# Optimization experiments

Measured on AMD Instinct MI355X. Metric: run time of the kernel, lower is better.

Reference implementation:

```python
import jax, jax.numpy as jnp
import numpy as np

N, D, H, C, K, NCLS, TW = 8192, 768, 4, 192, 8, 7, 1.0
HC = H * C  # 768


def setup_inputs() -> dict:
    key = jax.random.key(0)
    ks = jax.random.split(key, 40)
    gl = lambda i, shp: (jax.random.normal(ks[i], shp, jnp.float32)
                         * (1.0 / np.sqrt(shp[0] if len(shp) > 1 else shp[0])))
    inp = {"x": jax.random.normal(ks[0], (N, D), jnp.float32)}
    # BatchNorm (eval mode: running stats)
    inp["bn_gamma"] = jnp.ones((D,), jnp.float32)
    inp["bn_beta"] = jnp.zeros((D,), jnp.float32)
    inp["bn_rm"] = jnp.zeros((D,), jnp.float32)
    inp["bn_rv"] = jnp.ones((D,), jnp.float32)
    # GATConv params: W [in, H*C], att_src/att_dst [H, C], bias
    dims_in = [D, HC, HC, C]
    bias_dim = [HC, HC, C, C]  # concat,concat,mean,mean
    for li in range(4):
        b = 1 + li * 3
        inp[f"g{li+1}_w"] = gl(b, (dims_in[li], HC))
        inp[f"g{li+1}_as"] = jax.random.normal(ks[b + 1], (H, C), jnp.float32) * 0.1
        inp[f"g{li+1}_ad"] = jax.random.normal(ks[b + 2], (H, C), jnp.float32) * 0.1
        inp[f"g{li+1}_b"] = jnp.zeros((bias_dim[li],), jnp.float32)
    inp["res1_w"] = gl(14, (D, HC)); inp["res1_b"] = jnp.zeros((HC,), jnp.float32)
    inp["res2_w"] = gl(15, (HC, C)); inp["res2_b"] = jnp.zeros((C,), jnp.float32)
    for li, dim in zip(range(4), [HC, HC, C, C]):
        inp[f"ln{li+1}_g"] = jnp.ones((dim,), jnp.float32)
        inp[f"ln{li+1}_b"] = jnp.zeros((dim,), jnp.float32)
    inp["fc_w"] = gl(16, (C, NCLS)); inp["fc_b"] = jnp.zeros((NCLS,), jnp.float32)
    return inp


def _ln(x, g, b):
    mu = x.mean(-1, keepdims=True)
    v = ((x - mu) ** 2).mean(-1, keepdims=True)
    return (x - mu) * jax.lax.rsqrt(v + 1e-5) * g + b


def _build_edges(x):
    # cosine-similarity top-k graph (indices only; grads are cut upstream,
    # matching the original .item()-based host loop)
    xn = x / (jnp.linalg.norm(x, axis=1, keepdims=True) + 1e-8)
    sim = xn @ xn.T                       # [N, N]
    _, idx = jax.lax.top_k(sim, K + 1)    # first hit is self
    nbr = idx[:, 1:]                      # [N, K]
    src0 = jnp.repeat(jnp.arange(N), K)
    dst0 = nbr.reshape(-1)
    i = jnp.arange(N - 1)
    # temporal edges (i,i+1)&(i+1,i) added only if (i,i+1) not already a topk edge
    m = ~jnp.any(nbr[:-1] == (i + 1)[:, None], axis=1)
    sl = jnp.arange(N)  # self-loops (GATConv add_self_loops=True)
    src = jnp.concatenate([src0, i, i + 1, sl])
    dst = jnp.concatenate([dst0, i + 1, i, sl])
    mask = jnp.concatenate([jnp.ones(N * K, bool), m, m, jnp.ones(N, bool)])
    return src, dst, mask


def _gat(x, W, a_s, a_d, b, src, dst, mask, concat):
    n = x.shape[0]
    h = (x @ W).reshape(n, H, C)
    es = (h * a_s[None]).sum(-1)  # [N, H]
    ed = (h * a_d[None]).sum(-1)
    e = jax.nn.leaky_relu(es[src] + ed[dst], 0.2)  # [E, H]
    e = jnp.where(mask[:, None], e, -1e9)
    emax = jax.ops.segment_max(e, dst, num_segments=n)
    emax = jnp.where(jnp.isfinite(emax), emax, 0.0)
    ex = jnp.exp(e - emax[dst]) * mask[:, None].astype(e.dtype)
    denom = jax.ops.segment_sum(ex, dst, num_segments=n)
    alpha = ex / (denom[dst] + 1e-16)
    out = jax.ops.segment_sum(alpha[:, :, None] * h[src], dst, num_segments=n)
    out = out.reshape(n, HC) if concat else out.mean(1)
    return out + b


def reference(x, bn_gamma, bn_beta, bn_rm, bn_rv,
              g1_w, g1_as, g1_ad, g1_b, g2_w, g2_as, g2_ad, g2_b,
              g3_w, g3_as, g3_ad, g3_b, g4_w, g4_as, g4_ad, g4_b,
              res1_w, res1_b, res2_w, res2_b,
              ln1_g, ln1_b, ln2_g, ln2_b, ln3_g, ln3_b, ln4_g, ln4_b,
              fc_w, fc_b):
    xb = (x - bn_rm) * jax.lax.rsqrt(bn_rv + 1e-5) * bn_gamma + bn_beta
    src, dst, mask = _build_edges(jax.lax.stop_gradient(xb))
    r = xb @ res1_w + res1_b
    h = _gat(xb, g1_w, g1_as, g1_ad, g1_b, src, dst, mask, True)
    h = _ln(jax.nn.relu(h) + r, ln1_g, ln1_b)
    r = h
    h = _gat(h, g2_w, g2_as, g2_ad, g2_b, src, dst, mask, True)
    h = _ln(jax.nn.relu(h) + r, ln2_g, ln2_b)
    r = h @ res2_w + res2_b
    h = _gat(h, g3_w, g3_as, g3_ad, g3_b, src, dst, mask, False)
    h = _ln(jax.nn.relu(h) + r, ln3_g, ln3_b)
    r = h
    h = _gat(h, g4_w, g4_as, g4_ad, g4_b, src, dst, mask, False)
    h = _ln(jax.nn.relu(h) + r, ln4_g, ln4_b)
    return h @ fc_w + fc_b
```

## Files before the change

### kernel.cpp

```cpp
#include <hip/hip_runtime.h>
#include <hip/hip_bf16.h>

#define NN 8192
#define DD 768
#define HH 4
#define CC 192
#define KK 8
#define HC 768

typedef __attribute__((ext_vector_type(8))) short short8;
typedef __attribute__((ext_vector_type(4))) float floatx4;

static __device__ __forceinline__ short f2bf(float v) {
    unsigned u = __builtin_bit_cast(unsigned, v);
    u += 0x7fff + ((u >> 16) & 1);
    return (short)(u >> 16);
}
static __device__ __forceinline__ float bf2f(short s) {
    unsigned u = ((unsigned)(unsigned short)s) << 16;
    return __builtin_bit_cast(float, u);
}

static __device__ __forceinline__ void gl16(const void* g, void* l) {
    __builtin_amdgcn_global_load_lds(
        (__attribute__((address_space(1))) void*)(void*)g,
        (__attribute__((address_space(3))) void*)l, 16, 0, 0);
}

__global__ __launch_bounds__(256) void bnorm_kernel(const float* __restrict__ x,
    const float* __restrict__ g, const float* __restrict__ b,
    const float* __restrict__ rm, const float* __restrict__ rv,
    short* __restrict__ xbh, short* __restrict__ xbl,
    short* __restrict__ xnh, short* __restrict__ xnl)
{
    int i = blockIdx.x, t = threadIdx.x;
    __shared__ float red[256];
    float v[3];
    float ss = 0.f;
#pragma unroll
    for (int q = 0; q < 3; q++) {
        int d = t + q * 256;
        float xv = x[(size_t)i * DD + d];
        float vv = (xv - rm[d]) * rsqrtf(rv[d] + 1e-5f) * g[d] + b[d];
        v[q] = vv; ss += vv * vv;
    }
    red[t] = ss; __syncthreads();
    for (int s = 128; s; s >>= 1) { if (t < s) red[t] += red[t + s]; __syncthreads(); }
    float inv = 1.0f / (sqrtf(red[0]) + 1e-8f);
#pragma unroll
    for (int q = 0; q < 3; q++) {
        int d = t + q * 256;
        size_t idx = (size_t)i * DD + d;
        float vv = v[q];
        short h = f2bf(vv);
        xbh[idx] = h; xbl[idx] = f2bf(vv - bf2f(h));
        float nv = vv * inv;
        short nh = f2bf(nv);
        xnh[idx] = nh; xnl[idx] = f2bf(nv - bf2f(nh));
    }
}

__global__ __launch_bounds__(256) void wtrans(const float* __restrict__ w,
    short* __restrict__ whi, short* __restrict__ wlo, int K, int P)
{
    int idx = blockIdx.x * 256 + threadIdx.x;
    if (idx >= K * P) return;
    int p = idx / K, k = idx % K;
    float v = w[(size_t)k * P + p];
    short h = f2bf(v);
    whi[idx] = h;
    wlo[idx] = f2bf(v - bf2f(h));
}

__global__ __launch_bounds__(256) void mfma_nt(
    const short* __restrict__ Ahi, const short* __restrict__ Alo,
    const short* __restrict__ Bhi, const short* __restrict__ Blo,
    const float* __restrict__ bias, int biasN, float* __restrict__ C,
    int M, int K, int P, int Cstride)
{
    __shared__ __attribute__((aligned(16))) short sAh[128 * 32];
    __shared__ __attribute__((aligned(16))) short sAl[128 * 32];
    __shared__ __attribute__((aligned(16))) short sBh[128 * 32];
    __shared__ __attribute__((aligned(16))) short sBl[128 * 32];
    int t = threadIdx.x;
    int wave = t >> 6, lane = t & 63;
    int wm = wave & 1, wn = wave >> 1;
    int i0 = blockIdx.y * 128, j0 = blockIdx.x * 128;
    int mrow = lane & 15, quad = lane >> 4;

    int srow = lane >> 2;
    int kg   = (lane & 3) ^ ((lane >> 3) & 3);
    int koff = kg * 8;
    int c0 = wave * 2, c1 = c0 + 1;
    int ar0 = i0 + c0 * 16 + srow, ar1 = i0 + c1 * 16 + srow;
    int br0 = j0 + c0 * 16 + srow, br1 = j0 + c1 * 16 + srow;
    if (br0 > P - 1) br0 = P - 1;
    if (br1 > P - 1) br1 = P - 1;
    const short* pAh0 = Ahi + (size_t)ar0 * K + koff;
    const short* pAh1 = Ahi + (size_t)ar1 * K + koff;
    const short* pAl0 = Alo + (size_t)ar0 * K + koff;
    const short* pAl1 = Alo + (size_t)ar1 * K + koff;
    const short* pBh0 = Bhi + (size_t)br0 * K + koff;
    const short* pBh1 = Bhi + (size_t)br1 * K + koff;
    const short* pBl0 = Blo + (size_t)br0 * K + koff;
    const short* pBl1 = Blo + (size_t)br1 * K + koff;
    short* dA0 = sAh + c0 * 512; short* dA1 = sAh + c1 * 512;
    short* dAl0 = sAl + c0 * 512; short* dAl1 = sAl + c1 * 512;
    short* dB0 = sBh + c0 * 512; short* dB1 = sBh + c1 * 512;
    short* dBl0 = sBl + c0 * 512; short* dBl1 = sBl + c1 * 512;

    floatx4 acc[4][4];
#pragma unroll
    for (int a = 0; a < 4; a++)
#pragma unroll
        for (int b = 0; b < 4; b++) acc[a][b] = (floatx4){0.f, 0.f, 0.f, 0.f};

    int aoff[4], boff[4];
#pragma unroll
    for (int mt = 0; mt < 4; mt++) {
        int r = wm * 64 + mt * 16 + mrow;
        aoff[mt] = r * 32 + (quad ^ ((r >> 1) & 3)) * 8;
    }
#pragma unroll
    for (int nt = 0; nt < 4; nt++) {
        int r = wn * 64 + nt * 16 + mrow;
        boff[nt] = r * 32 + (quad ^ ((r >> 1) & 3)) * 8;
    }

    for (int k0 = 0; k0 < K; k0 += 32) {
        gl16(pAh0 + k0, dA0);  gl16(pAh1 + k0, dA1);
        gl16(pAl0 + k0, dAl0); gl16(pAl1 + k0, dAl1);
        gl16(pBh0 + k0, dB0);  gl16(pBh1 + k0, dB1);
        gl16(pBl0 + k0, dBl0); gl16(pBl1 + k0, dBl1);
        __syncthreads();

        short8 ah[4], al[4], bh[4], bl[4];
#pragma unroll
        for (int mt = 0; mt < 4; mt++) {
            ah[mt] = *(const short8*)(sAh + aoff[mt]);
            al[mt] = *(const short8*)(sAl + aoff[mt]);
        }
#pragma unroll
        for (int nt = 0; nt < 4; nt++) {
            bh[nt] = *(const short8*)(sBh + boff[nt]);
            bl[nt] = *(const short8*)(sBl + boff[nt]);
        }
#pragma unroll
        for (int mt = 0; mt < 4; mt++)
#pragma unroll
            for (int nt = 0; nt < 4; nt++) {
                acc[mt][nt] = __builtin_amdgcn_mfma_f32_16x16x32_bf16(
                    ah[mt], bh[nt], acc[mt][nt], 0, 0, 0);
                acc[mt][nt] = __builtin_amdgcn_mfma_f32_16x16x32_bf16(
                    ah[mt], bl[nt], acc[mt][nt], 0, 0, 0);
                acc[mt][nt] = __builtin_amdgcn_mfma_f32_16x16x32_bf16(
                    al[mt], bh[nt], acc[mt][nt], 0, 0, 0);
            }
        __syncthreads();
    }

#pragma unroll
    for (int mt = 0; mt < 4; mt++)
#pragma unroll
        for (int nt = 0; nt < 4; nt++) {
            int col = j0 + wn * 64 + nt * 16 + mrow;
            if (col < P) {
                float bb = (bias && col < biasN) ? bias[col] : 0.f;
#pragma unroll
                for (int r = 0; r < 4; r++) {
                    int row = i0 + wm * 64 + mt * 16 + quad * 4 + r;
                    C[(size_t)row * Cstride + col] = acc[mt][nt][r] + bb;
                }
            }
        }
}

__device__ __forceinline__ bool tk_try(float* v, int* id, float xv, int xi)
{
    if (xv > v[8] || (xv == v[8] && xi < id[8])) {
        v[8] = xv; id[8] = xi;
#pragma unroll
        for (int p = 8; p > 0; p--) {
            if (v[p] > v[p - 1] || (v[p] == v[p - 1] && id[p] < id[p - 1])) {
                float tv = v[p]; v[p] = v[p - 1]; v[p - 1] = tv;
                int ti2 = id[p]; id[p] = id[p - 1]; id[p - 1] = ti2;
            } else break;
        }
        return true;
    }
    return false;
}

__global__ __launch_bounds__(256) void topk1_kernel(const float* __restrict__ sim,
    float* __restrict__ pv, int* __restrict__ pi)
{
    int wave = threadIdx.x >> 6, lane = threadIdx.x & 63;
    int task = blockIdx.x * 4 + wave;
    int row = task >> 3, seg = task & 7;
    const float4* p4 = (const float4*)(sim + (size_t)row * NN + seg * 1024);

    float4 f0 = p4[lane], f1 = p4[lane + 64], f2 = p4[lane + 128], f3 = p4[lane + 192];
    float v[9]; int id[9];
#pragma unroll
    for (int q = 0; q < 9; q++) { v[q] = -3e38f; id[q] = 0x7fffffff; }
    int jb = seg * 1024 + lane * 4;
#pragma unroll
    for (int g = 0; g < 4; g++) {
        float4 f = g == 0 ? f0 : (g == 1 ? f1 : (g == 2 ? f2 : f3));
        float gm = fmaxf(fmaxf(f.x, f.y), fmaxf(f.z, f.w));
        if (gm >= v[8]) {
            int j = jb + g * 256;
            tk_try(v, id, f.x, j);
            tk_try(v, id, f.y, j + 1);
            tk_try(v, id, f.z, j + 2);
            tk_try(v, id, f.w, j + 3);
        }
    }
    float wv = -3e38f; int wi = 0x7fffffff;
#pragma unroll
    for (int r = 0; r < 9; r++) {
        float bv = v[0]; int bi = id[0];
#pragma unroll
        for (int off = 1; off < 64; off <<= 1) {
            float ov = __shfl_xor(bv, off);
            int oi = __shfl_xor(bi, off);
            if (ov > bv || (ov == bv && oi < bi)) { bv = ov; bi = oi; }
        }
        if (id[0] == bi) {
#pragma unroll
            for (int q = 0; q < 8; q++) { v[q] = v[q + 1]; id[q] = id[q + 1]; }
            v[8] = -3e38f; id[8] = 0x7fffffff;
        }
        if (lane == r) { wv = bv; wi = bi; }
    }
    if (lane < 9) {
        size_t o = (size_t)task * 9 + lane;
        pv[o] = wv; pi[o] = wi;
    }
}

__global__ __launch_bounds__(256) void topk2_kernel(const float* __restrict__ pv,
    const int* __restrict__ pi, int* __restrict__ nbr, int r0)
{
    int wave = threadIdx.x >> 6, lane = threadIdx.x & 63;
    int row = blockIdx.x * 4 + wave;
    size_t base = (size_t)row * 72;
    float v[2]; int id[2];
    v[0] = -3e38f; id[0] = 0x7fffffff;
    v[1] = -3e38f; id[1] = 0x7fffffff;
    if (lane < 72) { v[0] = pv[base + lane]; id[0] = pi[base + lane]; }
    if (lane < 8)  { v[1] = pv[base + 64 + lane]; id[1] = pi[base + 64 + lane]; }
    if (v[1] > v[0] || (v[1] == v[0] && id[1] < id[0])) {
        float tv = v[0]; v[0] = v[1]; v[1] = tv;
        int ti = id[0]; id[0] = id[1]; id[1] = ti;
    }
    int myi = 0;
#pragma unroll
    for (int r = 0; r < 9; r++) {
        float bv = v[0]; int bi = id[0];
#pragma unroll
        for (int off = 1; off < 64; off <<= 1) {
            float ov = __shfl_xor(bv, off);
            int oi = __shfl_xor(bi, off);
            if (ov > bv || (ov == bv && oi < bi)) { bv = ov; bi = oi; }
        }
        if (id[0] == bi) {
            v[0] = v[1]; id[0] = id[1];
            v[1] = -3e38f; id[1] = 0x7fffffff;
        }
        if (r >= 1 && lane == r - 1) myi = bi;
    }
    if (lane < KK) nbr[(size_t)(r0 + row) * KK + lane] = myi;
}

__global__ __launch_bounds__(256) void count_kernel(const int* __restrict__ nbr,
                                                    int* __restrict__ deg, int* __restrict__ mfl)
{
    int i = blockIdx.x * 256 + threadIdx.x;
    if (i >= NN) return;
    atomicAdd(&deg[i], 1);
    int mm = 0;
#pragma unroll
    for (int k = 0; k < KK; k++) {
        int j = nbr[i * KK + k];
        atomicAdd(&deg[j], 1);
        if (j == i + 1) mm = 1;
    }
    if (i < NN - 1) {
        mfl[i] = !mm;
        if (!mm) { atomicAdd(&deg[i + 1], 1); atomicAdd(&deg[i], 1); }
    }
}

__global__ __launch_bounds__(256) void scan_kernel(const int* __restrict__ deg,
                                                   int* __restrict__ rowptr, int* __restrict__ cur)
{
    __shared__ int sums[256];
    int t = threadIdx.x;
    int loc[32];
    int base = t * 32;
    int s = 0;
#pragma unroll
    for (int q = 0; q < 32; q++) { loc[q] = s; s += deg[base + q]; }
    sums[t] = s; __syncthreads();
    for (int off = 1; off < 256; off <<= 1) {
        int v = (t >= off) ? sums[t - off] : 0;
        __syncthreads();
        sums[t] += v;
        __syncthreads();
    }
    int myoff = (t == 0) ? 0 : sums[t - 1];
#pragma unroll
    for (int q = 0; q < 32; q++) { int rp = myoff + loc[q]; rowptr[base + q] = rp; cur[base + q] = rp; }
    if (t == 255) rowptr[NN] = sums[255];
}

__global__ __launch_bounds__(256) void fill_kernel(const int* __restrict__ nbr,
    const int* __restrict__ mfl, int* __restrict__ cur, int* __restrict__ csr)
{
    int i = blockIdx.x * 256 + threadIdx.x;
    if (i >= NN) return;
    int pos = atomicAdd(&cur[i], 1); csr[pos] = i;
#pragma unroll
    for (int k = 0; k < KK; k++) {
        int j = nbr[i * KK + k];
        pos = atomicAdd(&cur[j], 1); csr[pos] = i;
    }
    if (i < NN - 1 && mfl[i]) {
        pos = atomicAdd(&cur[i + 1], 1); csr[pos] = i;
        pos = atomicAdd(&cur[i], 1); csr[pos] = i + 1;
    }
}

__global__ __launch_bounds__(256) void esed_kernel(const float* __restrict__ h, int hst,
    const float* __restrict__ a_s, const float* __restrict__ a_d,
    float* __restrict__ es, float* __restrict__ ed)
{
    int i = blockIdx.x;
    int t = threadIdx.x;
    int w = t >> 6, lane = t & 63;
    const float* hr = h + (size_t)i * hst + w * CC;
    float ps = 0.f, pd = 0.f;
    for (int c = lane; c < CC; c += 64) {
        float x = hr[c];
        ps += x * a_s[w * CC + c];
        pd += x * a_d[w * CC + c];
    }
#pragma unroll
    for (int off = 32; off; off >>= 1) { ps += __shfl_down(ps, off); pd += __shfl_down(pd, off); }
    if (lane == 0) { es[i * HH + w] = ps; ed[i * HH + w] = pd; }
}

__global__ __launch_bounds__(256) void agg_ln_kernel(const float* __restrict__ h, int hst,
    const float* __restrict__ es, const float* __restrict__ ed,
    const int* __restrict__ rowptr, const int* __restrict__ csr,
    const float* __restrict__ gb, const float* __restrict__ rres, int rst,
    const float* __restrict__ gamma, const float* __restrict__ beta,
    float* __restrict__ outp, short* __restrict__ ohi, short* __restrict__ olo,
    int Dm, int concat,
    const float* __restrict__ fcw, const float* __restrict__ fcb,
    float* __restrict__ fco)
{
    int j = blockIdx.x;
    int t = threadIdx.x;
    int lane = t & 63, wave = t >> 6;
    __shared__ int ssrc[256];
    __shared__ float sal[256 * 4];
    __shared__ float sred[1024];
    __shared__ float accs[768];
    int p0 = rowptr[j], p1 = rowptr[j + 1];
    int cnt = p1 - p0;
    float edj[4];
#pragma unroll
    for (int hd = 0; hd < 4; hd++) edj[hd] = ed[j * 4 + hd];

    float acc0 = 0.f, acc1 = 0.f, acc2 = 0.f;
    int d0 = t, d1 = t + 256, d2 = t + 512;
    int h0 = d0 / CC, h1_ = d1 / CC, h2_ = d2 / CC;

    if (cnt <= 256) {
        float e[4];
        if (t < cnt) {
            int s = csr[p0 + t];
            ssrc[t] = s;
#pragma unroll
            for (int hd = 0; hd < 4; hd++) {
                float ee = es[s * 4 + hd] + edj[hd];
                e[hd] = ee > 0.f ? ee : 0.2f * ee;
            }
        } else {
#pragma unroll
            for (int hd = 0; hd < 4; hd++) e[hd] = -1e30f;
        }
        float mh[4];
#pragma unroll
        for (int hd = 0; hd < 4; hd++) {
            float rv = e[hd];
#pragma unroll
            for (int off = 32; off; off >>= 1) rv = fmaxf(rv, __shfl_down(rv, off));
            if (lane == 0) sred[wave * 4 + hd] = rv;
        }
        __syncthreads();
#pragma unroll
        for (int hd = 0; hd < 4; hd++)
            mh[hd] = fmaxf(fmaxf(sred[hd], sred[4 + hd]), fmaxf(sred[8 + hd], sred[12 + hd]));
        __syncthreads();
        float ex[4];
#pragma unroll
        for (int hd = 0; hd < 4; hd++) {
            ex[hd] = (t < cnt) ? expf(e[hd] - mh[hd]) : 0.f;
            float rv = ex[hd];
#pragma unroll
            for (int off = 32; off; off >>= 1) rv += __shfl_down(rv, off);
            if (lane == 0) sred[wave * 4 + hd] = rv;
        }
        __syncthreads();
#pragma unroll
        for (int hd = 0; hd < 4; hd++) {
            float dh = sred[hd] + sred[4 + hd] + sred[8 + hd] + sred[12 + hd] + 1e-16f;
            if (t < cnt) sal[t * 4 + hd] = ex[hd] / dh;
        }
        __syncthreads();
        for (int e2 = 0; e2 < cnt; e2++) {
            const float* hs = h + (size_t)ssrc[e2] * hst;
            acc0 += sal[e2 * 4 + h0] * hs[d0];
            acc1 += sal[e2 * 4 + h1_] * hs[d1];
            acc2 += sal[e2 * 4 + h2_] * hs[d2];
        }
    } else {
        float mh[4] = {-1e30f, -1e30f, -1e30f, -1e30f};
        for (int p = p0 + t; p < p1; p += 256) {
            int s = csr[p];
#pragma unroll
            for (int hd = 0; hd < 4; hd++) {
                float e = es[s * 4 + hd] + edj[hd];
                e = e > 0.f ? e : 0.2f * e;
                mh[hd] = fmaxf(mh[hd], e);
            }
        }
#pragma unroll
        for (int hd = 0; hd < 4; hd++) sred[hd * 256 + t] = mh[hd];
        __syncthreads();
        for (int s2 = 128; s2; s2 >>= 1) {
            if (t < s2)
#pragma unroll
                for (int hd = 0; hd < 4; hd++)
                    sred[hd * 256 + t] = fmaxf(sred[hd * 256 + t], sred[hd * 256 + t + s2]);
            __syncthreads();
        }
#pragma unroll
        for (int hd = 0; hd < 4; hd++) mh[hd] = sred[hd * 256];
        __syncthreads();
        float sh[4] = {0.f, 0.f, 0.f, 0.f};
        for (int p = p0 + t; p < p1; p += 256) {
            int s = csr[p];
#pragma unroll
            for (int hd = 0; hd < 4; hd++) {
                float e = es[s * 4 + hd] + edj[hd];
                e = e > 0.f ? e : 0.2f * e;
                sh[hd] += expf(e - mh[hd]);
            }
        }
#pragma unroll
        for (int hd = 0; hd < 4; hd++) sred[hd * 256 + t] = sh[hd];
        __syncthreads();
        for (int s2 = 128; s2; s2 >>= 1) {
            if (t < s2)
#pragma unroll
                for (int hd = 0; hd < 4; hd++)
                    sred[hd * 256 + t] += sred[hd * 256 + t + s2];
            __syncthreads();
        }
        float dh[4];
#pragma unroll
        for (int hd = 0; hd < 4; hd++) dh[hd] = sred[hd * 256] + 1e-16f;
        __syncthreads();
        for (int p = p0; p < p1; p += 64) {
            int cn = min(64, p1 - p);
            if (t < cn) {
                int s = csr[p + t];
                ssrc[t] = s;
#pragma unroll
                for (int hd = 0; hd < 4; hd++) {
                    float e = es[s * 4 + hd] + edj[hd];
                    e = e > 0.f ? e : 0.2f * e;
                    sal[t * 4 + hd] = expf(e - mh[hd]) / dh[hd];
                }
            }
            __syncthreads();
            for (int e2 = 0; e2 < cn; e2++) {
                const float* hs = h + (size_t)ssrc[e2] * hst;
                acc0 += sal[e2 * 4 + h0] * hs[d0];
                acc1 += sal[e2 * 4 + h1_] * hs[d1];
                acc2 += sal[e2 * 4 + h2_] * hs[d2];
            }
            __syncthreads();
        }
    }

    if (concat) {
        float v0 = fmaxf(acc0 + gb[d0], 0.f) + rres[(size_t)j * rst + d0];
        float v1 = fmaxf(acc1 + gb[d1], 0.f) + rres[(size_t)j * rst + d1];
        float v2 = fmaxf(acc2 + gb[d2], 0.f) + rres[(size_t)j * rst + d2];
        __syncthreads();
        sred[t] = v0 + v1 + v2; __syncthreads();
        for (int s = 128; s; s >>= 1) { if (t < s) sred[t] += sred[t + s]; __syncthreads(); }
        float mu = sred[0] / 768.f;
        __syncthreads();
        float a0 = v0 - mu, a1 = v1 - mu, a2 = v2 - mu;
        sred[t] = a0 * a0 + a1 * a1 + a2 * a2; __syncthreads();
        for (int s = 128; s; s >>= 1) { if (t < s) sred[t] += sred[t + s]; __syncthreads(); }
        float rs = rsqrtf(sred[0] / 768.f + 1e-5f);
        size_t base = (size_t)j * 768;
        float w0 = a0 * rs * gamma[d0] + beta[d0];
        float w1 = a1 * rs * gamma[d1] + beta[d1];
        float w2 = a2 * rs * gamma[d2] + beta[d2];
        outp[base + d0] = w0; outp[base + d1] = w1; outp[base + d2] = w2;
        short hh;
        hh = f2bf(w0); ohi[base + d0] = hh; olo[base + d0] = f2bf(w0 - bf2f(hh));
        hh = f2bf(w1); ohi[base + d1] = hh; olo[base + d1] = f2bf(w1 - bf2f(hh));
        hh = f2bf(w2); ohi[base + d2] = hh; olo[base + d2] = f2bf(w2 - bf2f(hh));
    } else {
        accs[d0] = acc0; accs[d1] = acc1; accs[d2] = acc2;
        __syncthreads();
        float val = 0.f;
        if (t < CC)
            val = fmaxf((accs[t] + accs[t + CC] + accs[t + 2 * CC] + accs[t + 3 * CC]) * 0.25f
                        + gb[t], 0.f) + rres[(size_t)j * rst + t];
        __syncthreads();
        sred[t] = (t < CC) ? val : 0.f; __syncthreads();
        for (int s = 128; s; s >>= 1) { if (t < s) sred[t] += sred[t + s]; __syncthreads(); }
        float mu = sred[0] / (float)CC;
        __syncthreads();
        float a = val - mu;
        sred[t] = (t < CC) ? a * a : 0.f; __syncthreads();
        for (int s = 128; s; s >>= 1) { if (t < s) sred[t] += sred[t + s]; __syncthreads(); }
        float rs = rsqrtf(sred[0] / (float)CC + 1e-5f);
        float w = a * rs * ((t < CC) ? gamma[t] : 0.f) + ((t < CC) ? beta[t] : 0.f);
        if (t < CC) {
            size_t idx = (size_t)j * CC + t;
            if (outp) outp[idx] = w;
            if (ohi) {
                short hh = f2bf(w);
                ohi[idx] = hh; olo[idx] = f2bf(w - bf2f(hh));
            }
            accs[t] = w;
        }
        if (fco) {
            __syncthreads();
            if (t < 64) {
#pragma unroll
                for (int n = 0; n < 7; n++) {
                    float p = 0.f;
                    for (int d = t; d < CC; d += 64) p += accs[d] * fcw[d * 7 + n];
#pragma unroll
                    for (int off = 32; off; off >>= 1) p += __shfl_down(p, off);
                    if (t == 0) fco[(size_t)j * 7 + n] = p + fcb[n];
                }
            }
        }
    }
}

extern "C" void kernel_launch(void* const* d_in, const int* in_sizes, int n_in,
                              void* d_out, int out_size, void* d_ws, size_t ws_size,
                              hipStream_t stream)
{
    const float* x     = (const float*)d_in[0];
    const float* bn_g  = (const float*)d_in[1];
    const float* bn_b  = (const float*)d_in[2];
    const float* bn_rm = (const float*)d_in[3];
    const float* bn_rv = (const float*)d_in[4];
    const float* g_w[4]  = {(const float*)d_in[5], (const float*)d_in[9],
                            (const float*)d_in[13], (const float*)d_in[17]};
    const float* g_as[4] = {(const float*)d_in[6], (const float*)d_in[10],
                            (const float*)d_in[14], (const float*)d_in[18]};
    const float* g_ad[4] = {(const float*)d_in[7], (const float*)d_in[11],
                            (const float*)d_in[15], (const float*)d_in[19]};
    const float* g_b[4]  = {(const float*)d_in[8], (const float*)d_in[12],
                            (const float*)d_in[16], (const float*)d_in[20]};
    const float* res1_w = (const float*)d_in[21];
    const float* res1_b = (const float*)d_in[22];
    const float* res2_w = (const float*)d_in[23];
    const float* res2_b = (const float*)d_in[24];
    const float* ln_g[4] = {(const float*)d_in[25], (const float*)d_in[27],
                            (const float*)d_in[29], (const float*)d_in[31]};
    const float* ln_b[4] = {(const float*)d_in[26], (const float*)d_in[28],
                            (const float*)d_in[30], (const float*)d_in[32]};
    const float* fc_w = (const float*)d_in[33];
    const float* fc_b = (const float*)d_in[34];
    float* out = (float*)d_out;

    float* F = (float*)d_ws;
    float* ASIM = F; F += 16777216;
    float* H1   = F; F += 6291456;
    float* HB24 = F; F += 6291456;
    float* H2   = F; F += 6291456;
    float* H3   = F; F += 1572864;
    float* ES   = F; F += 32768;
    float* ED   = F; F += 32768;
    short* S = (short*)F;
    short* XNH = S; S += 6291456;
    short* XNL = S; S += 6291456;
    short* XAH = S; S += 6291456;
    short* XAL = S; S += 6291456;
    short* WT1H = S; S += 1179648;
    short* WT1L = S; S += 1179648;
    short* WT2H = S; S += 589824;
    short* WT2L = S; S += 589824;
    short* WT3H = S; S += 737280;
    short* WT3L = S; S += 737280;
    short* WT4H = S; S += 147456;
    short* WT4L = S; S += 147456;
    int* I = (int*)S;
    int* NBR    = I; I += NN * KK;
    int* DEG    = I; I += NN;
    int* ROWPTR = I; I += NN + 8;
    int* CUR    = I; I += NN;
    int* MFL    = I; I += NN;
    int* CSR    = I; I += 131072;
    float* PV   = (float*)I; I += 147456;
    int* PI     = I; I += 147456;

    bnorm_kernel<<<NN, 256, 0, stream>>>(x, bn_g, bn_b, bn_rm, bn_rv,
                                         XAH, XAL, XNH, XNL);
    wtrans<<<(DD * HC + 255) / 256, 256, 0, stream>>>(res1_w, WT1H, WT1L, DD, HC);
    wtrans<<<(DD * HC + 255) / 256, 256, 0, stream>>>(g_w[0], WT1H + 768 * 768, WT1L + 768 * 768, DD, HC);
    wtrans<<<(HC * HC + 255) / 256, 256, 0, stream>>>(g_w[1], WT2H, WT2L, HC, HC);
    wtrans<<<(HC * CC + 255) / 256, 256, 0, stream>>>(res2_w, WT3H, WT3L, HC, CC);
    wtrans<<<(HC * HC + 255) / 256, 256, 0, stream>>>(g_w[2], WT3H + 192 * 768, WT3L + 192 * 768, HC, HC);
    wtrans<<<(CC * HC + 255) / 256, 256, 0, stream>>>(g_w[3], WT4H, WT4L, CC, HC);
    for (int ch = 0; ch < 4; ch++) {
        mfma_nt<<<dim3(NN / 128, 2048 / 128), 256, 0, stream>>>(
            XNH + (size_t)ch * 2048 * DD, XNL + (size_t)ch * 2048 * DD,
            XNH, XNL, nullptr, 0, ASIM, 2048, DD, NN, NN);
        topk1_kernel<<<4096, 256, 0, stream>>>(ASIM, PV, PI);
        topk2_kernel<<<512, 256, 0, stream>>>(PV, PI, NBR, ch * 2048);
    }
    hipMemsetAsync(DEG, 0, NN * sizeof(int), stream);
    count_kernel<<<NN / 256, 256, 0, stream>>>(NBR, DEG, MFL);
    scan_kernel<<<1, 256, 0, stream>>>(DEG, ROWPTR, CUR);
    fill_kernel<<<NN / 256, 256, 0, stream>>>(NBR, MFL, CUR, CSR);
    float* HB1 = ASIM;
    mfma_nt<<<dim3(12, NN / 128), 256, 0, stream>>>(XAH, XAL, WT1H, WT1L,
        res1_b, 768, HB1, NN, DD, 1536, 1536);
    esed_kernel<<<NN, 256, 0, stream>>>(HB1 + 768, 1536, g_as[0], g_ad[0], ES, ED);
    agg_ln_kernel<<<NN, 256, 0, stream>>>(HB1 + 768, 1536, ES, ED, ROWPTR, CSR,
        g_b[0], HB1, 1536, ln_g[0], ln_b[0], H1, XAH, XAL, HC, 1, nullptr, nullptr, nullptr);
    mfma_nt<<<dim3(6, NN / 128), 256, 0, stream>>>(XAH, XAL, WT2H, WT2L,
        nullptr, 0, HB24, NN, HC, HC, HC);
    esed_kernel<<<NN, 256, 0, stream>>>(HB24, HC, g_as[1], g_ad[1], ES, ED);
    agg_ln_kernel<<<NN, 256, 0, stream>>>(HB24, HC, ES, ED, ROWPTR, CSR,
        g_b[1], H1, HC, ln_g[1], ln_b[1], H2, XAH, XAL, HC, 1, nullptr, nullptr, nullptr);
    float* HB3 = ASIM;
    mfma_nt<<<dim3(8, NN / 128), 256, 0, stream>>>(XAH, XAL, WT3H, WT3L,
        res2_b, 192, HB3, NN, HC, 960, 960);
    esed_kernel<<<NN, 256, 0, stream>>>(HB3 + 192, 960, g_as[2], g_ad[2], ES, ED);
    agg_ln_kernel<<<NN, 256, 0, stream>>>(HB3 + 192, 960, ES, ED, ROWPTR, CSR,
        g_b[2], HB3, 960, ln_g[2], ln_b[2], H3, XAH, XAL, CC, 0, nullptr, nullptr, nullptr);
    mfma_nt<<<dim3(6, NN / 128), 256, 0, stream>>>(XAH, XAL, WT4H, WT4L,
        nullptr, 0, HB24, NN, CC, HC, HC);
    esed_kernel<<<NN, 256, 0, stream>>>(HB24, HC, g_as[3], g_ad[3], ES, ED);
    agg_ln_kernel<<<NN, 256, 0, stream>>>(HB24, HC, ES, ED, ROWPTR, CSR,
        g_b[3], H3, CC, ln_g[3], ln_b[3], nullptr, nullptr, nullptr, CC, 0, fc_w, fc_b, out);
}
```

Baseline: 1.224 ms.

## Fuse similarity GEMM with per-tile top-k and merge weight transposes

The cosine-similarity GEMM now does a per-128-column-tile top-9 selection in its epilogue through shared memory, so the full NxN similarity matrix is never written to or re-read from global memory. The four chunked GEMM/topk1/topk2 launches become one fused kernel plus one final merge over 64 tile candidates per row. Six weight-transpose launches are also merged into a single kernel. The cost is a heavier epilogue, with serialized shuffle-based reductions per row inside the GEMM, and a larger candidate merge in topk2.

```diff
diff --git a/kernel.cpp b/kernel.cpp
--- a/kernel.cpp
+++ b/kernel.cpp
@@ -60,16 +60,28 @@
     }
 }
 
-__global__ __launch_bounds__(256) void wtrans(const float* __restrict__ w,
-    short* __restrict__ whi, short* __restrict__ wlo, int K, int P)
+__global__ __launch_bounds__(256) void wtrans6(
+    const float* w0, short* o0h, short* o0l,
+    const float* w1, short* o1h, short* o1l,
+    const float* w2, short* o2h, short* o2l,
+    const float* w3, short* o3h, short* o3l,
+    const float* w4, short* o4h, short* o4l,
+    const float* w5, short* o5h, short* o5l)
 {
     int idx = blockIdx.x * 256 + threadIdx.x;
-    if (idx >= K * P) return;
-    int p = idx / K, k = idx % K;
+    const float* w; short* oh; short* ol; int K, P; int r;
+    if (idx < 589824)            { w = w0; oh = o0h; ol = o0l; K = 768; P = 768; r = idx; }
+    else if (idx < 2 * 589824)   { w = w1; oh = o1h; ol = o1l; K = 768; P = 768; r = idx - 589824; }
+    else if (idx < 3 * 589824)   { w = w2; oh = o2h; ol = o2l; K = 768; P = 768; r = idx - 2 * 589824; }
+    else if (idx < 3 * 589824 + 147456) { w = w3; oh = o3h; ol = o3l; K = 768; P = 192; r = idx - 3 * 589824; }
+    else if (idx < 4 * 589824 + 147456) { w = w4; oh = o4h; ol = o4l; K = 768; P = 768; r = idx - 3 * 589824 - 147456; }
+    else if (idx < 4 * 589824 + 2 * 147456) { w = w5; oh = o5h; ol = o5l; K = 192; P = 768; r = idx - 4 * 589824 - 147456; }
+    else return;
+    int p = r / K, k = r % K;
     float v = w[(size_t)k * P + p];
     short h = f2bf(v);
-    whi[idx] = h;
-    wlo[idx] = f2bf(v - bf2f(h));
+    oh[r] = h;
+    ol[r] = f2bf(v - bf2f(h));
 }
 
 __global__ __launch_bounds__(256) void mfma_nt(
@@ -175,48 +187,148 @@
         }
 }
 
-__device__ __forceinline__ bool tk_try(float* v, int* id, float xv, int xi)
-{
-    if (xv > v[8] || (xv == v[8] && xi < id[8])) {
-        v[8] = xv; id[8] = xi;
-#pragma unroll
-        for (int p = 8; p > 0; p--) {
-            if (v[p] > v[p - 1] || (v[p] == v[p - 1] && id[p] < id[p - 1])) {
-                float tv = v[p]; v[p] = v[p - 1]; v[p - 1] = tv;
-                int ti2 = id[p]; id[p] = id[p - 1]; id[p - 1] = ti2;
-            } else break;
-        }
-        return true;
-    }
-    return false;
-}
-
-__global__ __launch_bounds__(256) void topk1_kernel(const float* __restrict__ sim,
+__global__ __launch_bounds__(256) void mfma_topk(
+    const short* __restrict__ Xh, const short* __restrict__ Xl,
     float* __restrict__ pv, int* __restrict__ pi)
 {
+    __shared__ __attribute__((aligned(16))) short smem[16384];
+    short* sAh = smem;
+    short* sAl = smem + 4096;
+    short* sBh = smem + 8192;
+    short* sBl = smem + 12288;
+    int t = threadIdx.x;
+    int wave = t >> 6, lane = t & 63;
+    int wm = wave & 1, wn = wave >> 1;
+    int i0 = blockIdx.y * 128, j0 = blockIdx.x * 128;
+    int mrow = lane & 15, quad = lane >> 4;
+
+    int srow = lane >> 2;
+    int kg   = (lane & 3) ^ ((lane >> 3) & 3);
+    int koff = kg * 8;
+    int c0 = wave * 2, c1 = c0 + 1;
+    int ar0 = i0 + c0 * 16 + srow, ar1 = i0 + c1 * 16 + srow;
+    int br0 = j0 + c0 * 16 + srow, br1 = j0 + c1 * 16 + srow;
+    const short* pAh0 = Xh + (size_t)ar0 * DD + koff;
+    const short* pAh1 = Xh + (size_t)ar1 * DD + koff;
+    const short* pAl0 = Xl + (size_t)ar0 * DD + koff;
+    const short* pAl1 = Xl + (size_t)ar1 * DD + koff;
+    const short* pBh0 = Xh + (size_t)br0 * DD + koff;
+    const short* pBh1 = Xh + (size_t)br1 * DD + koff;
+    const short* pBl0 = Xl + (size_t)br0 * DD + koff;
+    const short* pBl1 = Xl + (size_t)br1 * DD + koff;
+    short* dA0 = sAh + c0 * 512; short* dA1 = sAh + c1 * 512;
+    short* dAl0 = sAl + c0 * 512; short* dAl1 = sAl + c1 * 512;
+    short* dB0 = sBh + c0 * 512; short* dB1 = sBh + c1 * 512;
+    short* dBl0 = sBl + c0 * 512; short* dBl1 = sBl + c1 * 512;
+
+    floatx4 acc[4][4];
+#pragma unroll
+    for (int a = 0; a < 4; a++)
+#pragma unroll
+        for (int b = 0; b < 4; b++) acc[a][b] = (floatx4){0.f, 0.f, 0.f, 0.f};
+
+    int aoff[4], boff[4];
+#pragma unroll
+    for (int mt = 0; mt < 4; mt++) {
+        int r = wm * 64 + mt * 16 + mrow;
+        aoff[mt] = r * 32 + (quad ^ ((r >> 1) & 3)) * 8;
+    }
+#pragma unroll
+    for (int nt = 0; nt < 4; nt++) {
+        int r = wn * 64 + nt * 16 + mrow;
+        boff[nt] = r * 32 + (quad ^ ((r >> 1) & 3)) * 8;
+    }
+
+    for (int k0 = 0; k0 < DD; k0 += 32) {
+        gl16(pAh0 + k0, dA0);  gl16(pAh1 + k0, dA1);
+        gl16(pAl0 + k0, dAl0); gl16(pAl1 + k0, dAl1);
+        gl16(pBh0 + k0, dB0);  gl16(pBh1 + k0, dB1);
+        gl16(pBl0 + k0, dBl0); gl16(pBl1 + k0, dBl1);
+        __syncthreads();
+
+        short8 ah[4], al[4], bh[4], bl[4];
+#pragma unroll
+        for (int mt = 0; mt < 4; mt++) {
+            ah[mt] = *(const short8*)(sAh + aoff[mt]);
+            al[mt] = *(const short8*)(sAl + aoff[mt]);
+        }
+#pragma unroll
+        for (int nt = 0; nt < 4; nt++) {
+            bh[nt] = *(const short8*)(sBh + boff[nt]);
+            bl[nt] = *(const short8*)(sBl + boff[nt]);
+        }
+#pragma unroll
+        for (int mt = 0; mt < 4; mt++)
+#pragma unroll
+            for (int nt = 0; nt < 4; nt++) {
+                acc[mt][nt] = __builtin_amdgcn_mfma_f32_16x16x32_bf16(
+                    ah[mt], bh[nt], acc[mt][nt], 0, 0, 0);
+                acc[mt][nt] = __builtin_amdgcn_mfma_f32_16x16x32_bf16(
+                    ah[mt], bl[nt], acc[mt][nt], 0, 0, 0);
+                acc[mt][nt] = __builtin_amdgcn_mfma_f32_16x16x32_bf16(
+                    al[mt], bh[nt], acc[mt][nt], 0, 0, 0);
+            }
+        __syncthreads();
+    }
+
+    float* fl = (float*)smem;
+    for (int half = 0; half < 2; half++) {
+        __syncthreads();
+        if (wm == half) {
+#pragma unroll
+            for (int mt = 0; mt < 4; mt++)
+#pragma unroll
+                for (int nt = 0; nt < 4; nt++)
+#pragma unroll
+                    for (int r = 0; r < 4; r++)
+                        fl[(mt * 16 + quad * 4 + r) * 128 + wn * 64 + nt * 16 + mrow]
+                            = acc[mt][nt][r];
+        }
+        __syncthreads();
+        for (int rr = 0; rr < 16; rr++) {
+            int lrow = wave * 16 + rr;
+            float va = fl[lrow * 128 + lane];
+            float vb = fl[lrow * 128 + lane + 64];
+            int ia = j0 + lane, ib = j0 + lane + 64;
+            if (vb > va || (vb == va && ib < ia)) {
+                float tv = va; va = vb; vb = tv;
+                int ti = ia; ia = ib; ib = ti;
+            }
+            float ov_ = 0.f; int oi_ = 0;
+#pragma unroll
+            for (int r = 0; r < 9; r++) {
+                float bv = va; int bi = ia;
+#pragma unroll
+                for (int off = 1; off < 64; off <<= 1) {
+                    float w = __shfl_xor(bv, off);
+                    int wi = __shfl_xor(bi, off);
+                    if (w > bv || (w == bv && wi < bi)) { bv = w; bi = wi; }
+                }
+                if (ia == bi) { va = vb; ia = ib; vb = -3e38f; ib = 0x7fffffff; }
+                if (lane == r) { ov_ = bv; oi_ = bi; }
+            }
+            if (lane < 9) {
+                int grow = i0 + half * 64 + lrow;
+                size_t pos = (size_t)grow * 576 + (size_t)lane * 64 + blockIdx.x;
+                pv[pos] = ov_; pi[pos] = oi_;
+            }
+        }
+    }
+}
+
+__global__ __launch_bounds__(256) void topk2_kernel(const float* __restrict__ pv,
+    const int* __restrict__ pi, int* __restrict__ nbr)
+{
     int wave = threadIdx.x >> 6, lane = threadIdx.x & 63;
-    int task = blockIdx.x * 4 + wave;
-    int row = task >> 3, seg = task & 7;
-    const float4* p4 = (const float4*)(sim + (size_t)row * NN + seg * 1024);
-
-    float4 f0 = p4[lane], f1 = p4[lane + 64], f2 = p4[lane + 128], f3 = p4[lane + 192];
+    int row = blockIdx.x * 4 + wave;
+    size_t base = (size_t)row * 576;
     float v[9]; int id[9];
 #pragma unroll
-    for (int q = 0; q < 9; q++) { v[q] = -3e38f; id[q] = 0x7fffffff; }
-    int jb = seg * 1024 + lane * 4;
-#pragma unroll
-    for (int g = 0; g < 4; g++) {
-        float4 f = g == 0 ? f0 : (g == 1 ? f1 : (g == 2 ? f2 : f3));
-        float gm = fmaxf(fmaxf(f.x, f.y), fmaxf(f.z, f.w));
-        if (gm >= v[8]) {
-            int j = jb + g * 256;
-            tk_try(v, id, f.x, j);
-            tk_try(v, id, f.y, j + 1);
-            tk_try(v, id, f.z, j + 2);
-            tk_try(v, id, f.w, j + 3);
-        }
-    }
-    float wv = -3e38f; int wi = 0x7fffffff;
+    for (int q = 0; q < 9; q++) {
+        size_t pos = base + (size_t)q * 64 + lane;
+        v[q] = pv[pos]; id[q] = pi[pos];
+    }
+    int myi = 0;
 #pragma unroll
     for (int r = 0; r < 9; r++) {
         float bv = v[0]; int bi = id[0];
@@ -231,46 +343,9 @@
             for (int q = 0; q < 8; q++) { v[q] = v[q + 1]; id[q] = id[q + 1]; }
             v[8] = -3e38f; id[8] = 0x7fffffff;
         }
-        if (lane == r) { wv = bv; wi = bi; }
-    }
-    if (lane < 9) {
-        size_t o = (size_t)task * 9 + lane;
-        pv[o] = wv; pi[o] = wi;
-    }
-}
-
-__global__ __launch_bounds__(256) void topk2_kernel(const float* __restrict__ pv,
-    const int* __restrict__ pi, int* __restrict__ nbr, int r0)
-{
-    int wave = threadIdx.x >> 6, lane = threadIdx.x & 63;
-    int row = blockIdx.x * 4 + wave;
-    size_t base = (size_t)row * 72;
-    float v[2]; int id[2];
-    v[0] = -3e38f; id[0] = 0x7fffffff;
-    v[1] = -3e38f; id[1] = 0x7fffffff;
-    if (lane < 72) { v[0] = pv[base + lane]; id[0] = pi[base + lane]; }
-    if (lane < 8)  { v[1] = pv[base + 64 + lane]; id[1] = pi[base + 64 + lane]; }
-    if (v[1] > v[0] || (v[1] == v[0] && id[1] < id[0])) {
-        float tv = v[0]; v[0] = v[1]; v[1] = tv;
-        int ti = id[0]; id[0] = id[1]; id[1] = ti;
-    }
-    int myi = 0;
-#pragma unroll
-    for (int r = 0; r < 9; r++) {
-        float bv = v[0]; int bi = id[0];
-#pragma unroll
-        for (int off = 1; off < 64; off <<= 1) {
-            float ov = __shfl_xor(bv, off);
-            int oi = __shfl_xor(bi, off);
-            if (ov > bv || (ov == bv && oi < bi)) { bv = ov; bi = oi; }
-        }
-        if (id[0] == bi) {
-            v[0] = v[1]; id[0] = id[1];
-            v[1] = -3e38f; id[1] = 0x7fffffff;
-        }
         if (r >= 1 && lane == r - 1) myi = bi;
     }
-    if (lane < KK) nbr[(size_t)(r0 + row) * KK + lane] = myi;
+    if (lane < KK) nbr[(size_t)row * KK + lane] = myi;
 }
 
 __global__ __launch_bounds__(256) void count_kernel(const int* __restrict__ nbr,
@@ -619,24 +694,20 @@
     int* CUR    = I; I += NN;
     int* MFL    = I; I += NN;
     int* CSR    = I; I += 131072;
-    float* PV   = (float*)I; I += 147456;
-    int* PI     = I; I += 147456;
+    float* PV = ASIM;
+    int*   PI = (int*)(ASIM + 4718592);
 
     bnorm_kernel<<<NN, 256, 0, stream>>>(x, bn_g, bn_b, bn_rm, bn_rv,
                                          XAH, XAL, XNH, XNL);
-    wtrans<<<(DD * HC + 255) / 256, 256, 0, stream>>>(res1_w, WT1H, WT1L, DD, HC);
-    wtrans<<<(DD * HC + 255) / 256, 256, 0, stream>>>(g_w[0], WT1H + 768 * 768, WT1L + 768 * 768, DD, HC);
-    wtrans<<<(HC * HC + 255) / 256, 256, 0, stream>>>(g_w[1], WT2H, WT2L, HC, HC);
-    wtrans<<<(HC * CC + 255) / 256, 256, 0, stream>>>(res2_w, WT3H, WT3L, HC, CC);
-    wtrans<<<(HC * HC + 255) / 256, 256, 0, stream>>>(g_w[2], WT3H + 192 * 768, WT3L + 192 * 768, HC, HC);
-    wtrans<<<(CC * HC + 255) / 256, 256, 0, stream>>>(g_w[3], WT4H, WT4L, CC, HC);
-    for (int ch = 0; ch < 4; ch++) {
-        mfma_nt<<<dim3(NN / 128, 2048 / 128), 256, 0, stream>>>(
-            XNH + (size_t)ch * 2048 * DD, XNL + (size_t)ch * 2048 * DD,
-            XNH, XNL, nullptr, 0, ASIM, 2048, DD, NN, NN);
-        topk1_kernel<<<4096, 256, 0, stream>>>(ASIM, PV, PI);
-        topk2_kernel<<<512, 256, 0, stream>>>(PV, PI, NBR, ch * 2048);
-    }
+    wtrans6<<<(4 * 589824 + 2 * 147456 + 255) / 256, 256, 0, stream>>>(
+        res1_w, WT1H, WT1L,
+        g_w[0], WT1H + 768 * 768, WT1L + 768 * 768,
+        g_w[1], WT2H, WT2L,
+        res2_w, WT3H, WT3L,
+        g_w[2], WT3H + 192 * 768, WT3L + 192 * 768,
+        g_w[3], WT4H, WT4L);
+    mfma_topk<<<dim3(64, 64), 256, 0, stream>>>(XNH, XNL, PV, PI);
+    topk2_kernel<<<NN / 4, 256, 0, stream>>>(PV, PI, NBR);
     hipMemsetAsync(DEG, 0, NN * sizeof(int), stream);
     count_kernel<<<NN / 256, 256, 0, stream>>>(NBR, DEG, MFL);
     scan_kernel<<<1, 256, 0, stream>>>(DEG, ROWPTR, CUR);
```

After: 2.189 ms. +78.9%, slower.

## Fuse attention-score dots into GEMM epilogue, store GAT features as bf16

Applied to the files above, without the earlier changes.

Computes the per-head source/destination attention dot products inside the GEMM epilogue, using shuffle reductions and atomicAdd into zeroed per-layer buffers, which removes the separate esed kernels. The GAT projected features are written as bf16, so the gather in the aggregation kernel reads half the bytes. Residual outputs go to separate fp32 buffers. The six weight-transpose launches are merged into one kernel, and an unused fp32 layer-2 output store is skipped. Storing features in bf16 lowers aggregation precision, and the atomics make the summation order nondeterministic.

```diff
diff --git a/kernel.cpp b/kernel.cpp
--- a/kernel.cpp
+++ b/kernel.cpp
@@ -60,23 +60,39 @@
     }
 }
 
-__global__ __launch_bounds__(256) void wtrans(const float* __restrict__ w,
-    short* __restrict__ whi, short* __restrict__ wlo, int K, int P)
+__global__ __launch_bounds__(256) void wtrans6(
+    const float* w0, short* o0h, short* o0l,
+    const float* w1, short* o1h, short* o1l,
+    const float* w2, short* o2h, short* o2l,
+    const float* w3, short* o3h, short* o3l,
+    const float* w4, short* o4h, short* o4l,
+    const float* w5, short* o5h, short* o5l)
 {
     int idx = blockIdx.x * 256 + threadIdx.x;
-    if (idx >= K * P) return;
-    int p = idx / K, k = idx % K;
+    const float* w; short* oh; short* ol; int K, P; int r;
+    if (idx < 589824)            { w = w0; oh = o0h; ol = o0l; K = 768; P = 768; r = idx; }
+    else if (idx < 2 * 589824)   { w = w1; oh = o1h; ol = o1l; K = 768; P = 768; r = idx - 589824; }
+    else if (idx < 3 * 589824)   { w = w2; oh = o2h; ol = o2l; K = 768; P = 768; r = idx - 2 * 589824; }
+    else if (idx < 3 * 589824 + 147456) { w = w3; oh = o3h; ol = o3l; K = 768; P = 192; r = idx - 3 * 589824; }
+    else if (idx < 4 * 589824 + 147456) { w = w4; oh = o4h; ol = o4l; K = 768; P = 768; r = idx - 3 * 589824 - 147456; }
+    else if (idx < 4 * 589824 + 2 * 147456) { w = w5; oh = o5h; ol = o5l; K = 192; P = 768; r = idx - 4 * 589824 - 147456; }
+    else return;
+    int p = r / K, k = r % K;
     float v = w[(size_t)k * P + p];
     short h = f2bf(v);
-    whi[idx] = h;
-    wlo[idx] = f2bf(v - bf2f(h));
+    oh[r] = h;
+    ol[r] = f2bf(v - bf2f(h));
 }
 
 __global__ __launch_bounds__(256) void mfma_nt(
     const short* __restrict__ Ahi, const short* __restrict__ Alo,
     const short* __restrict__ Bhi, const short* __restrict__ Blo,
-    const float* __restrict__ bias, int biasN, float* __restrict__ C,
-    int M, int K, int P, int Cstride)
+    const float* __restrict__ bias, int biasN,
+    float* __restrict__ C, int Cstride,
+    short* __restrict__ Cbf, int bfoff, int bfstride,
+    const float* __restrict__ a_s, const float* __restrict__ a_d,
+    float* __restrict__ es, float* __restrict__ ed, int hoff,
+    int M, int K, int P)
 {
     __shared__ __attribute__((aligned(16))) short sAh[128 * 32];
     __shared__ __attribute__((aligned(16))) short sAl[128 * 32];
@@ -165,14 +181,61 @@
         for (int nt = 0; nt < 4; nt++) {
             int col = j0 + wn * 64 + nt * 16 + mrow;
             if (col < P) {
-                float bb = (bias && col < biasN) ? bias[col] : 0.f;
-#pragma unroll
-                for (int r = 0; r < 4; r++) {
-                    int row = i0 + wm * 64 + mt * 16 + quad * 4 + r;
-                    C[(size_t)row * Cstride + col] = acc[mt][nt][r] + bb;
+                if (col < bfoff) {
+                    float bb = (bias && col < biasN) ? bias[col] : 0.f;
+#pragma unroll
+                    for (int r = 0; r < 4; r++) {
+                        int row = i0 + wm * 64 + mt * 16 + quad * 4 + r;
+                        C[(size_t)row * Cstride + col] = acc[mt][nt][r] + bb;
+                    }
+                } else {
+#pragma unroll
+                    for (int r = 0; r < 4; r++) {
+                        int row = i0 + wm * 64 + mt * 16 + quad * 4 + r;
+                        Cbf[(size_t)row * bfstride + col - bfoff] = f2bf(acc[mt][nt][r]);
+                    }
                 }
             }
         }
+
+    if (a_s) {
+        int base = j0 + wn * 64;
+        if (base >= hoff && base + 64 <= P) {
+            int head = (base - hoff) / CC;
+            int cb = (base - hoff) % CC;
+#pragma unroll
+            for (int mt = 0; mt < 4; mt++) {
+                float ps[4] = {0.f, 0.f, 0.f, 0.f};
+                float pd[4] = {0.f, 0.f, 0.f, 0.f};
+#pragma unroll
+                for (int nt = 0; nt < 4; nt++) {
+                    int c = cb + nt * 16 + mrow;
+                    float as_ = a_s[head * CC + c];
+                    float ad_ = a_d[head * CC + c];
+#pragma unroll
+                    for (int r = 0; r < 4; r++) {
+                        ps[r] += acc[mt][nt][r] * as_;
+                        pd[r] += acc[mt][nt][r] * ad_;
+                    }
+                }
+#pragma unroll
+                for (int off = 1; off < 16; off <<= 1)
+#pragma unroll
+                    for (int r = 0; r < 4; r++) {
+                        ps[r] += __shfl_xor(ps[r], off);
+                        pd[r] += __shfl_xor(pd[r], off);
+                    }
+                if (mrow == 0) {
+#pragma unroll
+                    for (int r = 0; r < 4; r++) {
+                        int row = i0 + wm * 64 + mt * 16 + quad * 4 + r;
+                        atomicAdd(&es[row * 4 + head], ps[r]);
+                        atomicAdd(&ed[row * 4 + head], pd[r]);
+                    }
+                }
+            }
+        }
+    }
 }
 
 __device__ __forceinline__ bool tk_try(float* v, int* id, float xv, int xi)
@@ -332,26 +395,7 @@
     }
 }
 
-__global__ __launch_bounds__(256) void esed_kernel(const float* __restrict__ h, int hst,
-    const float* __restrict__ a_s, const float* __restrict__ a_d,
-    float* __restrict__ es, float* __restrict__ ed)
-{
-    int i = blockIdx.x;
-    int t = threadIdx.x;
-    int w = t >> 6, lane = t & 63;
-    const float* hr = h + (size_t)i * hst + w * CC;
-    float ps = 0.f, pd = 0.f;
-    for (int c = lane; c < CC; c += 64) {
-        float x = hr[c];
-        ps += x * a_s[w * CC + c];
-        pd += x * a_d[w * CC + c];
-    }
-#pragma unroll
-    for (int off = 32; off; off >>= 1) { ps += __shfl_down(ps, off); pd += __shfl_down(pd, off); }
-    if (lane == 0) { es[i * HH + w] = ps; ed[i * HH + w] = pd; }
-}
-
-__global__ __launch_bounds__(256) void agg_ln_kernel(const float* __restrict__ h, int hst,
+__global__ __launch_bounds__(256) void agg_ln_kernel(const short* __restrict__ h, int hst,
     const float* __restrict__ es, const float* __restrict__ ed,
     const int* __restrict__ rowptr, const int* __restrict__ csr,
     const float* __restrict__ gb, const float* __restrict__ rres, int rst,
@@ -422,10 +466,10 @@
         }
         __syncthreads();
         for (int e2 = 0; e2 < cnt; e2++) {
-            const float* hs = h + (size_t)ssrc[e2] * hst;
-            acc0 += sal[e2 * 4 + h0] * hs[d0];
-            acc1 += sal[e2 * 4 + h1_] * hs[d1];
-            acc2 += sal[e2 * 4 + h2_] * hs[d2];
+            const short* hs = h + (size_t)ssrc[e2] * hst;
+            acc0 += sal[e2 * 4 + h0] * bf2f(hs[d0]);
+            acc1 += sal[e2 * 4 + h1_] * bf2f(hs[d1]);
+            acc2 += sal[e2 * 4 + h2_] * bf2f(hs[d2]);
         }
     } else {
         float mh[4] = {-1e30f, -1e30f, -1e30f, -1e30f};
@@ -489,10 +533,10 @@
             }
             __syncthreads();
             for (int e2 = 0; e2 < cn; e2++) {
-                const float* hs = h + (size_t)ssrc[e2] * hst;
-                acc0 += sal[e2 * 4 + h0] * hs[d0];
-                acc1 += sal[e2 * 4 + h1_] * hs[d1];
-                acc2 += sal[e2 * 4 + h2_] * hs[d2];
+                const short* hs = h + (size_t)ssrc[e2] * hst;
+                acc0 += sal[e2 * 4 + h0] * bf2f(hs[d0]);
+                acc1 += sal[e2 * 4 + h1_] * bf2f(hs[d1]);
+                acc2 += sal[e2 * 4 + h2_] * bf2f(hs[d2]);
             }
             __syncthreads();
         }
@@ -515,7 +559,7 @@
         float w0 = a0 * rs * gamma[d0] + beta[d0];
         float w1 = a1 * rs * gamma[d1] + beta[d1];
         float w2 = a2 * rs * gamma[d2] + beta[d2];
-        outp[base + d0] = w0; outp[base + d1] = w1; outp[base + d2] = w2;
+        if (outp) { outp[base + d0] = w0; outp[base + d1] = w1; outp[base + d2] = w2; }
         short hh;
         hh = f2bf(w0); ohi[base + d0] = hh; olo[base + d0] = f2bf(w0 - bf2f(hh));
         hh = f2bf(w1); ohi[base + d1] = hh; olo[base + d1] = f2bf(w1 - bf2f(hh));
@@ -593,17 +637,17 @@
 
     float* F = (float*)d_ws;
     float* ASIM = F; F += 16777216;
+    float* R1   = F; F += 6291456;
     float* H1   = F; F += 6291456;
-    float* HB24 = F; F += 6291456;
-    float* H2   = F; F += 6291456;
+    float* R2   = F; F += 1572864;
     float* H3   = F; F += 1572864;
-    float* ES   = F; F += 32768;
-    float* ED   = F; F += 32768;
+    float* ESB  = F; F += 262144;
     short* S = (short*)F;
     short* XNH = S; S += 6291456;
     short* XNL = S; S += 6291456;
     short* XAH = S; S += 6291456;
     short* XAL = S; S += 6291456;
+    short* HBH = S; S += 6291456;
     short* WT1H = S; S += 1179648;
     short* WT1L = S; S += 1179648;
     short* WT2H = S; S += 589824;
@@ -621,46 +665,49 @@
     int* CSR    = I; I += 131072;
     float* PV   = (float*)I; I += 147456;
     int* PI     = I; I += 147456;
+    float* ES[4], *ED[4];
+    for (int l = 0; l < 4; l++) { ES[l] = ESB + l * 65536; ED[l] = ES[l] + 32768; }
 
     bnorm_kernel<<<NN, 256, 0, stream>>>(x, bn_g, bn_b, bn_rm, bn_rv,
                                          XAH, XAL, XNH, XNL);
-    wtrans<<<(DD * HC + 255) / 256, 256, 0, stream>>>(res1_w, WT1H, WT1L, DD, HC);
-    wtrans<<<(DD * HC + 255) / 256, 256, 0, stream>>>(g_w[0], WT1H + 768 * 768, WT1L + 768 * 768, DD, HC);
-    wtrans<<<(HC * HC + 255) / 256, 256, 0, stream>>>(g_w[1], WT2H, WT2L, HC, HC);
-    wtrans<<<(HC * CC + 255) / 256, 256, 0, stream>>>(res2_w, WT3H, WT3L, HC, CC);
-    wtrans<<<(HC * HC + 255) / 256, 256, 0, stream>>>(g_w[2], WT3H + 192 * 768, WT3L + 192 * 768, HC, HC);
-    wtrans<<<(CC * HC + 255) / 256, 256, 0, stream>>>(g_w[3], WT4H, WT4L, CC, HC);
+    hipMemsetAsync(ESB, 0, 262144 * sizeof(float), stream);
+    hipMemsetAsync(DEG, 0, NN * sizeof(int), stream);
+    wtrans6<<<(4 * 589824 + 2 * 147456 + 255) / 256, 256, 0, stream>>>(
+        res1_w, WT1H, WT1L,
+        g_w[0], WT1H + 768 * 768, WT1L + 768 * 768,
+        g_w[1], WT2H, WT2L,
+        res2_w, WT3H, WT3L,
+        g_w[2], WT3H + 192 * 768, WT3L + 192 * 768,
+        g_w[3], WT4H, WT4L);
     for (int ch = 0; ch < 4; ch++) {
         mfma_nt<<<dim3(NN / 128, 2048 / 128), 256, 0, stream>>>(
             XNH + (size_t)ch * 2048 * DD, XNL + (size_t)ch * 2048 * DD,
-            XNH, XNL, nullptr, 0, ASIM, 2048, DD, NN, NN);
+            XNH, XNL, nullptr, 0, ASIM, NN, nullptr, 0x7fffffff, 0,
+            nullptr, nullptr, nullptr, nullptr, 0, 2048, DD, NN);
         topk1_kernel<<<4096, 256, 0, stream>>>(ASIM, PV, PI);
         topk2_kernel<<<512, 256, 0, stream>>>(PV, PI, NBR, ch * 2048);
     }
-    hipMemsetAsync(DEG, 0, NN * sizeof(int), stream);
     count_kernel<<<NN / 256, 256, 0, stream>>>(NBR, DEG, MFL);
     scan_kernel<<<1, 256, 0, stream>>>(DEG, ROWPTR, CUR);
     fill_kernel<<<NN / 256, 256, 0, stream>>>(NBR, MFL, CUR, CSR);
-    float* HB1 = ASIM;
     mfma_nt<<<dim3(12, NN / 128), 256, 0, stream>>>(XAH, XAL, WT1H, WT1L,
-        res1_b, 768, HB1, NN, DD, 1536, 1536);
-    esed_kernel<<<NN, 256, 0, stream>>>(HB1 + 768, 1536, g_as[0], g_ad[0], ES, ED);
-    agg_ln_kernel<<<NN, 256, 0, stream>>>(HB1 + 768, 1536, ES, ED, ROWPTR, CSR,
-        g_b[0], HB1, 1536, ln_g[0], ln_b[0], H1, XAH, XAL, HC, 1, nullptr, nullptr, nullptr);
+        res1_b, 768, R1, 768, HBH, 768, 768,
+        g_as[0], g_ad[0], ES[0], ED[0], 768, NN, DD, 1536);
+    agg_ln_kernel<<<NN, 256, 0, stream>>>(HBH, 768, ES[0], ED[0], ROWPTR, CSR,
+        g_b[0], R1, 768, ln_g[0], ln_b[0], H1, XAH, XAL, HC, 1, nullptr, nullptr, nullptr);
     mfma_nt<<<dim3(6, NN / 128), 256, 0, stream>>>(XAH, XAL, WT2H, WT2L,
-        nullptr, 0, HB24, NN, HC, HC, HC);
-    esed_kernel<<<NN, 256, 0, stream>>>(HB24, HC, g_as[1], g_ad[1], ES, ED);
-    agg_ln_kernel<<<NN, 256, 0, stream>>>(HB24, HC, ES, ED, ROWPTR, CSR,
-        g_b[1], H1, HC, ln_g[1], ln_b[1], H2, XAH, XAL, HC, 1, nullptr, nullptr, nullptr);
-    float* HB3 = ASIM;
+        nullptr, 0, nullptr, 0, HBH, 0, 768,
+        g_as[1], g_ad[1], ES[1], ED[1], 0, NN, HC, HC);
+    agg_ln_kernel<<<NN, 256, 0, stream>>>(HBH, 768, ES[1], ED[1], ROWPTR, CSR,
+        g_b[1], H1, 768, ln_g[1], ln_b[1], nullptr, XAH, XAL, HC, 1, nullptr, nullptr, nullptr);
     mfma_nt<<<dim3(8, NN / 128), 256, 0, stream>>>(XAH, XAL, WT3H, WT3L,
-        res2_b, 192, HB3, NN, HC, 960, 960);
-    esed_kernel<<<NN, 256, 0, stream>>>(HB3 + 192, 960, g_as[2], g_ad[2], ES, ED);
-    agg_ln_kernel<<<NN, 256, 0, stream>>>(HB3 + 192, 960, ES, ED, ROWPTR, CSR,
-        g_b[2], HB3, 960, ln_g[2], ln_b[2], H3, XAH, XAL, CC, 0, nullptr, nullptr, nullptr);
+        res2_b, 192, R2, 192, HBH, 192, 768,
+        g_as[2], g_ad[2], ES[2], ED[2], 192, NN, HC, 960);
+    agg_ln_kernel<<<NN, 256, 0, stream>>>(HBH, 768, ES[2], ED[2], ROWPTR, CSR,
+        g_b[2], R2, 192, ln_g[2], ln_b[2], H3, XAH, XAL, CC, 0, nullptr, nullptr, nullptr);
     mfma_nt<<<dim3(6, NN / 128), 256, 0, stream>>>(XAH, XAL, WT4H, WT4L,
-        nullptr, 0, HB24, NN, CC, HC, HC);
-    esed_kernel<<<NN, 256, 0, stream>>>(HB24, HC, g_as[3], g_ad[3], ES, ED);
-    agg_ln_kernel<<<NN, 256, 0, stream>>>(HB24, HC, ES, ED, ROWPTR, CSR,
-        g_b[3], H3, CC, ln_g[3], ln_b[3], nullptr, nullptr, nullptr, CC, 0, fc_w, fc_b, out);
-}
+        nullptr, 0, nullptr, 0, HBH, 0, 768,
+        g_as[3], g_ad[3], ES[3], ED[3], 0, NN, CC, HC);
+    agg_ln_kernel<<<NN, 256, 0, stream>>>(HBH, 768, ES[3], ED[3], ROWPTR, CSR,
+        g_b[3], H3, 192, ln_g[3], ln_b[3], nullptr, nullptr, nullptr, CC, 0, fc_w, fc_b, out);
+}
```

Result: no change. 1.208 ms (-1.3%).
